# Kernel tuning notes

Measured on AMD Instinct MI355X. Metric: run time of the kernel, lower is better.

The kernel has to match this reference:

```python
import jax, jax.numpy as jnp
import numpy as np

B, S, N, D = 4, 12, 716, 64
H = 4            # num_heads
ALPHA = 0.2      # LeakyReLU negative slope
NEG = -9e15      # mask fill value from the torch code (-9000000000000000.0)


def setup_inputs() -> dict:
    key = jax.random.key(0)
    ks = jax.random.split(key, 20)
    sc = 1.0 / np.sqrt(D)
    inputs = jax.random.normal(ks[0], (B, S, N, D), dtype=jnp.float32)
    adj = jax.random.randint(ks[1], (N, N), 0, 2).astype(jnp.int32)
    in_degree = jax.random.randint(ks[2], (N,), 0, N)
    out_degree = jax.random.randint(ks[3], (N,), 0, N)
    # embeddings with padding_idx=0 -> row 0 zeroed
    in_emb = (jax.random.normal(ks[4], (N, D)) * sc).at[0].set(0.0)
    out_emb = (jax.random.normal(ks[5], (N, D)) * sc).at[0].set(0.0)
    # GAT params
    W = jax.random.normal(ks[6], (D, D)) * sc
    a1 = jax.random.normal(ks[7], (D, 1)) * sc
    a2 = jax.random.normal(ks[8], (D, 1)) * sc
    # spatial multi-head attention params
    Wq = jax.random.normal(ks[9], (D, D)) * sc
    bq = jnp.zeros((D,))
    Wk = jax.random.normal(ks[10], (D, D)) * sc
    bk = jnp.zeros((D,))
    Wv = jax.random.normal(ks[11], (D, D)) * sc
    bv = jnp.zeros((D,))
    Wo = jax.random.normal(ks[12], (D, D)) * sc
    bo = jnp.zeros((D,))
    # pred_linear: 2D -> D
    Wp = jax.random.normal(ks[13], (2 * D, D)) * (1.0 / np.sqrt(2 * D))
    bp = jnp.zeros((D,))
    return dict(inputs=inputs, adj=adj, in_degree=in_degree, out_degree=out_degree,
                in_emb=in_emb, out_emb=out_emb, W=W, a1=a1, a2=a2,
                Wq=Wq, bq=bq, Wk=Wk, bk=bk, Wv=Wv, bv=bv, Wo=Wo, bo=bo,
                Wp=Wp, bp=bp)


def reference(inputs, adj, in_degree, out_degree, in_emb, out_emb,
              W, a1, a2, Wq, bq, Wk, bk, Wv, bv, Wo, bo, Wp, bp):
    b, s, n, d = inputs.shape
    dh = d // H
    # degree embeddings, broadcast over batch & time: [N, D]
    spatial_emb = in_emb[in_degree] + out_emb[out_degree]

    # ---- GAT, vectorized over all batch*seq samples (orig loops per sample) ----
    x = inputs.reshape(b * s, n, d)
    Wh = jnp.einsum('bnd,de->bne', x, W)                 # [BS, N, D]
    Wh1 = Wh @ a1                                        # [BS, N, 1]
    Wh2 = Wh @ a2                                        # [BS, N, 1]
    e = Wh1 + jnp.swapaxes(Wh2, 1, 2)                    # [BS, N, N]
    e = jnp.where(e > 0, e, ALPHA * e)                   # LeakyReLU
    e = jnp.where(adj[None] > 0, e, NEG)                 # adjacency mask
    attn = jax.nn.softmax(e, axis=-1)                    # softmax(dim=1) on 2D == last axis
    out1 = jax.nn.elu(attn @ Wh).reshape(b, s, n, d)     # dropout is identity in eval

    # ---- Spatial multi-head attention over nodes ----
    y = inputs + spatial_emb                             # [B, S, N, D]
    q = (y @ Wq + bq).reshape(b, s, n, H, dh)
    k = (y @ Wk + bk).reshape(b, s, n, H, dh)
    v = (y @ Wv + bv).reshape(b, s, n, H, dh)
    scores = jnp.einsum('bsnhk,bsmhk->bshnm', q, k) / jnp.sqrt(jnp.float32(dh))
    p = jax.nn.softmax(scores, axis=-1)                  # [B, S, H, N, N]
    o = jnp.einsum('bshnm,bsmhk->bsnhk', p, v).reshape(b, s, n, d)
    out2 = o @ Wo + bo

    # ---- fuse and project ----
    return jnp.concatenate([out1, out2], axis=-1) @ Wp + bp
```

## Files before the change

kernel.cpp:

```cpp
#include <hip/hip_runtime.h>
#include <hip/hip_bf16.h>

#define BN   716
#define BD   64
#define BH   4
#define BDH  16
#define BBS  48
#define NCH  23
#define NJT  45

typedef __hip_bfloat16 bf16;
typedef __attribute__((ext_vector_type(8))) short short8;
typedef __attribute__((ext_vector_type(4))) short s16x4;
typedef __attribute__((ext_vector_type(4))) float f32x4;

__device__ __forceinline__ float b2f(bf16 x){ return __bfloat162float(x); }
__device__ __forceinline__ bf16 f2b(float x){ return __float2bfloat16(x); }
__device__ __forceinline__ short bfbits(float x){
  union { bf16 h; short s; } c; c.h = __float2bfloat16(x); return c.s;
}
__device__ __forceinline__ unsigned packbf(float a, float b){
  unsigned ua = __float_as_uint(a) + 0x8000u;
  unsigned ub = __float_as_uint(b) + 0x8000u;
  return __builtin_amdgcn_perm(ub, ua, 0x07060302u);
}
__device__ __forceinline__ short8 pack8(float a,float b,float c,float d,
                                        float e,float f,float g,float h){
  short8 r; r[0]=bfbits(a); r[1]=bfbits(b); r[2]=bfbits(c); r[3]=bfbits(d);
  r[4]=bfbits(e); r[5]=bfbits(f); r[6]=bfbits(g); r[7]=bfbits(h); return r;
}

#define MFMA16(a,b,c) __builtin_amdgcn_mfma_f32_16x16x32_bf16(a,b,c,0,0,0)

#if __has_builtin(__builtin_amdgcn_mfma_f32_16x16x16_bf16)
#define HAVE_MFMA16K 1
__device__ __forceinline__ f32x4 mfma16k(s16x4 a, s16x4 b, f32x4 c){
  return __builtin_amdgcn_mfma_f32_16x16x16_bf16(a, b, c, 0, 0, 0);
}
#elif __has_builtin(__builtin_amdgcn_mfma_f32_16x16x16bf16_1k)
#define HAVE_MFMA16K 1
__device__ __forceinline__ f32x4 mfma16k(s16x4 a, s16x4 b, f32x4 c){
  return __builtin_amdgcn_mfma_f32_16x16x16bf16_1k(a, b, c, 0, 0, 0);
}
#else
#define HAVE_MFMA16K 0
#endif

__global__ __launch_bounds__(256) void k_prep(
    const int* __restrict__ adj,
    const float* __restrict__ W,  const float* __restrict__ Wq,
    const float* __restrict__ Wk, const float* __restrict__ Wv,
    const float* __restrict__ Wo, const float* __restrict__ bo,
    const float* __restrict__ Wp, const float* __restrict__ bp,
    unsigned* __restrict__ mask, bf16* __restrict__ WB,
    bf16* __restrict__ WF, float* __restrict__ bfuse)
{
  int b = blockIdx.x, t = threadIdx.x;
  if (b < 65){
    int w = b * 256 + t;
    if (w < BN * NCH){
      int row = w / NCH, wc = w - row * NCH;
      unsigned m = 0;
      int jb = wc * 32;
      for (int bb = 0; bb < 32; bb++){
        int j = jb + bb;
        if (j < BN && adj[(long)row * BN + j] > 0) m |= (1u << bb);
      }
      mask[w] = m;
    }
  } else if (b < 69){
#pragma unroll
    for (int i = 0; i < 16; i++){
      int idx = (b - 65) * 4096 + i * 256 + t;
      int n = idx >> 6, kk = idx & 63;
      const float* src = (n < 64) ? W : (n < 128) ? Wq : (n < 192) ? Wk : Wv;
      WB[idx] = f2b(src[kk * BD + (n & 63)]);
    }
  } else if (b < 101){
    int idx = (b - 69) * 256 + t;
    int n = idx >> 7, kk = idx & 127;
    float v;
    if (kk < 64){
      v = Wp[kk * BD + n];
    } else {
      v = 0.f;
      int r = kk - 64;
      for (int m = 0; m < BD; m++)
        v += Wo[r * BD + m] * Wp[(BD + m) * BD + n];
    }
    WF[idx] = f2b(v);
  } else {
    if (t < BD){
      float acc = bp[t];
      for (int m = 0; m < BD; m++)
        acc += bo[m] * Wp[(BD + m) * BD + t];
      bfuse[t] = acc;
    }
  }
}

__global__ __launch_bounds__(256) void k_proj(
    const float* __restrict__ x,
    const int* __restrict__ ind, const int* __restrict__ outd,
    const float* __restrict__ in_emb, const float* __restrict__ out_emb,
    const float* __restrict__ a1p, const float* __restrict__ a2p,
    const bf16* __restrict__ WB,
    const float* __restrict__ bq, const float* __restrict__ bk, const float* __restrict__ bv,
    bf16* __restrict__ WhS, float* __restrict__ Wh1, float* __restrict__ Wh2,
    bf16* __restrict__ Qt, bf16* __restrict__ Kt, bf16* __restrict__ Vt16)
{
  __shared__ short st[64][72];
  int bs = blockIdx.x, tile = blockIdx.y;
  int n0 = tile * 64;
  int t = threadIdx.x, w = t >> 6, lane = t & 63, quad = lane >> 4, l15 = lane & 15;
  long sb = (long)bs * BN;
  int rowi = n0 + w * 16 + l15;
  int rc = rowi < BN ? rowi : BN - 1;
  const float* xr  = x + (sb + rc) * BD;
  const float* ier = in_emb  + (long)ind [rc] * BD;
  const float* oer = out_emb + (long)outd[rc] * BD;

  f32x4 aw[4], aqkv[12];
#pragma unroll
  for (int i2 = 0; i2 < 4;  i2++) aw[i2]   = (f32x4){0,0,0,0};
#pragma unroll
  for (int i2 = 0; i2 < 12; i2++) aqkv[i2] = (f32x4){0,0,0,0};

#pragma unroll
  for (int kc = 0; kc < 2; kc++){
    int k0 = kc * 32 + quad * 8;
    float4 xa = *(const float4*)(xr  + k0);
    float4 xb = *(const float4*)(xr  + k0 + 4);
    float4 ia = *(const float4*)(ier + k0);
    float4 ib = *(const float4*)(ier + k0 + 4);
    float4 oa = *(const float4*)(oer + k0);
    float4 ob = *(const float4*)(oer + k0 + 4);
    short8 ax = pack8(xa.x, xa.y, xa.z, xa.w, xb.x, xb.y, xb.z, xb.w);
    short8 ay = pack8(xa.x+ia.x+oa.x, xa.y+ia.y+oa.y, xa.z+ia.z+oa.z, xa.w+ia.w+oa.w,
                      xb.x+ib.x+ob.x, xb.y+ib.y+ob.y, xb.z+ib.z+ob.z, xb.w+ib.w+ob.w);
#pragma unroll
    for (int nt = 0; nt < 4; nt++)
      aw[nt] = MFMA16(ax, *(const short8*)(WB + (nt*16 + l15) * BD + k0), aw[nt]);
#pragma unroll
    for (int nt = 0; nt < 12; nt++)
      aqkv[nt] = MFMA16(ay, *(const short8*)(WB + (64 + nt*16 + l15) * BD + k0), aqkv[nt]);
  }

  {
    float s1v[4] = {0,0,0,0}, s2v[4] = {0,0,0,0};
#pragma unroll
    for (int nt = 0; nt < 4; nt++){
      float a1f = a1p[nt*16 + l15], a2f = a2p[nt*16 + l15];
#pragma unroll
      for (int reg = 0; reg < 4; reg++){
        s1v[reg] += aw[nt][reg] * a1f;
        s2v[reg] += aw[nt][reg] * a2f;
      }
    }
#pragma unroll
    for (int off = 1; off < 16; off <<= 1){
#pragma unroll
      for (int reg = 0; reg < 4; reg++){
        s1v[reg] += __shfl_xor(s1v[reg], off);
        s2v[reg] += __shfl_xor(s2v[reg], off);
      }
    }
    if (l15 == 0){
#pragma unroll
      for (int reg = 0; reg < 4; reg++){
        int rr = n0 + w*16 + quad*4 + reg;
        if (rr < BN){ Wh1[sb + rr] = s1v[reg]; Wh2[sb + rr] = s2v[reg]; }
      }
    }
  }

#pragma unroll
  for (int nt = 0; nt < 4; nt++)
    *(short4*)&st[nt*16 + l15][w*16 + quad*4] = make_short4(
        bfbits(aw[nt][0]), bfbits(aw[nt][1]), bfbits(aw[nt][2]), bfbits(aw[nt][3]));
  __syncthreads();
#pragma unroll
  for (int s = 0; s < 2; s++){
    int L = (t*2 + s) * 8;
    int kb = L & 31, d = (L >> 5) & 63, chl = L >> 11;
    int ch = tile * 2 + chl;
    if (ch < NCH)
      *(uint4*)(WhS + (((long)bs*NCH + ch)*64 + d)*32 + kb) = *(const uint4*)&st[d][chl*32 + kb];
  }
  __syncthreads();

#pragma unroll
  for (int nt = 0; nt < 4; nt++){
    float bb = bv[nt*16 + l15];
    *(short4*)&st[nt*16 + l15][w*16 + quad*4] = make_short4(
        bfbits(aqkv[8+nt][0]+bb), bfbits(aqkv[8+nt][1]+bb),
        bfbits(aqkv[8+nt][2]+bb), bfbits(aqkv[8+nt][3]+bb));
  }
  __syncthreads();
  {
    int jl = t >> 6;
    int c  = t & 15, qq = (t >> 4) & 3;
    int jt = tile * 4 + jl;
    if (jt < NJT){
#pragma unroll
      for (int h = 0; h < BH; h++){
        s16x4 v4 = *(const s16x4*)&st[h*16 + c][jl*16 + qq*4];
        *(s16x4*)(Vt16 + ((((long)bs*BH + h)*NJT + jt)*64 + (t & 63))*4) = v4;
      }
    }
  }
  __syncthreads();

#pragma unroll
  for (int nt = 0; nt < 4; nt++){
    float bb = bq[nt*16 + l15];
#pragma unroll
    for (int reg = 0; reg < 4; reg++)
      st[w*16 + quad*4 + reg][nt*16 + l15] = bfbits((aqkv[nt][reg] + bb) * 0.25f);
  }
  __syncthreads();
#pragma unroll
  for (int s = 0; s < 2; s++){
    int L = (t*2 + s) * 8;
    int kb = L & 15, nl = (L >> 4) & 63, h = L >> 10;
    int jt = tile * 4 + (nl >> 4);
    if (jt < NJT)
      *(uint4*)(Qt + ((((long)bs*BH + h)*NJT + jt)*16 + (nl&15))*16 + kb)
          = *(const uint4*)&st[nl][h*16 + kb];
  }
  __syncthreads();

#pragma unroll
  for (int nt = 0; nt < 4; nt++){
    float bb = bk[nt*16 + l15];
#pragma unroll
    for (int reg = 0; reg < 4; reg++)
      st[w*16 + quad*4 + reg][nt*16 + l15] = bfbits(aqkv[4+nt][reg] + bb);
  }
  __syncthreads();
#pragma unroll
  for (int s = 0; s < 2; s++){
    int L = (t*2 + s) * 8;
    int kb = L & 15, nl = (L >> 4) & 63, h = L >> 10;
    int jt = tile * 4 + (nl >> 4);
    if (jt < NJT)
      *(uint4*)(Kt + ((((long)bs*BH + h)*NJT + jt)*16 + (nl&15))*16 + kb)
          = *(const uint4*)&st[nl][h*16 + kb];
  }
}

__global__ __launch_bounds__(256) void k_attn(
    const float* __restrict__ Wh1, const float* __restrict__ Wh2,
    const unsigned* __restrict__ mask, const bf16* __restrict__ WhS,
    const bf16* __restrict__ Qt, const bf16* __restrict__ Kt,
    const bf16* __restrict__ Vt16,
    bf16* __restrict__ out1, bf16* __restrict__ o)
{
#if !HAVE_MFMA16K
  __shared__ short pw[4][16][48];
#endif
  int bs = blockIdx.x, yb = blockIdx.y;
  int t = threadIdx.x, w = t >> 6, lane = t & 63, quad = lane >> 4, l15 = lane & 15;
  long sb = (long)bs * BN;

  if (yb < 12){
    int rt = yb * 4 + w;
    if (rt >= NJT) return;
    int i = rt * 16 + l15;
    int ic = i < BN ? i : BN - 1;
    float e1 = Wh1[sb + ic];
    const unsigned* mrow = mask + (long)ic * NCH;
    const float* w2 = Wh2 + sb;

    float sl = 0.f;
    f32x4 acc0 = {0,0,0,0}, acc1 = {0,0,0,0}, acc2 = {0,0,0,0}, acc3 = {0,0,0,0};
    for (int ch = 0; ch < NCH; ch++){
      int j0 = ch * 32 + quad * 8;
      unsigned m8 = (mrow[ch] >> (quad * 8)) & 0xFFu;
      float4 wa  = *(const float4*)(w2 + j0);
      float4 wb4 = *(const float4*)(w2 + j0 + 4);
      float sv[8] = {wa.x, wa.y, wa.z, wa.w, wb4.x, wb4.y, wb4.z, wb4.w};
      float p[8];
#pragma unroll
      for (int jj = 0; jj < 8; jj++){
        float e = e1 + sv[jj];
        e = (e > 0.f) ? e : 0.2f * e;
        float pp = ((m8 >> jj) & 1u) ? __expf(e) : 0.f;
        sl += pp;
        p[jj] = pp;
      }
      union { unsigned u[4]; short8 v; } A;
      A.u[0] = packbf(p[0], p[1]); A.u[1] = packbf(p[2], p[3]);
      A.u[2] = packbf(p[4], p[5]); A.u[3] = packbf(p[6], p[7]);
      const bf16* wbp = WhS + ((long)bs*NCH + ch)*2048 + quad * 8;
      acc0 = MFMA16(A.v, *(const short8*)(wbp + ( 0 + l15) * 32), acc0);
      acc1 = MFMA16(A.v, *(const short8*)(wbp + (16 + l15) * 32), acc1);
      acc2 = MFMA16(A.v, *(const short8*)(wbp + (32 + l15) * 32), acc2);
      acc3 = MFMA16(A.v, *(const short8*)(wbp + (48 + l15) * 32), acc3);
    }
    sl += __shfl_xor(sl, 16);
    sl += __shfl_xor(sl, 32);
    float inv[4];
#pragma unroll
    for (int reg = 0; reg < 4; reg++){
      int srcl = quad * 4 + reg;
      float s = __int_as_float(__builtin_amdgcn_ds_bpermute(srcl << 2, __float_as_int(sl)));
      inv[reg] = 1.0f / s;
    }
    const f32x4* accs[4] = {&acc0, &acc1, &acc2, &acc3};
#pragma unroll
    for (int nt = 0; nt < 4; nt++){
#pragma unroll
      for (int reg = 0; reg < 4; reg++){
        int gi = rt * 16 + quad * 4 + reg;
        if (gi < BN){
          float val = (*accs[nt])[reg] * inv[reg];
          val = (val > 0.f) ? val : (__expf(val) - 1.f);
          out1[(sb + gi) * BD + nt*16 + l15] = f2b(val);
        }
      }
    }
    return;
  }

  int rt = yb - 12, h = w;
  const bf16* Qh = Qt   + ((long)bs*BH + h) * NJT * 256;
  const bf16* Kh = Kt   + ((long)bs*BH + h) * NJT * 256;
  const bf16* Vh = Vt16 + ((long)bs*BH + h) * NJT * 256;

  short8 bq = {0,0,0,0,0,0,0,0};
  if (quad < 2) bq = *(const short8*)(Qh + rt*256 + l15*16 + quad*8);

  f32x4 oacc = {0,0,0,0};
  float psum = 0.f;

#if HAVE_MFMA16K
#pragma unroll 3
  for (int jt = 0; jt < NJT; jt++){
    short8 ak = {0,0,0,0,0,0,0,0};
    if (quad < 2) ak = *(const short8*)(Kh + jt*256 + l15*16 + quad*8);
    f32x4 c = MFMA16(ak, bq, ((f32x4){0,0,0,0}));
    bool inval = (jt == NJT-1) && (quad == 3);
    float p[4];
#pragma unroll
    for (int reg = 0; reg < 4; reg++){
      float pp = __expf(c[reg]);
      pp = inval ? 0.f : pp;
      psum += pp;
      p[reg] = pp;
    }
    union { unsigned u[2]; s16x4 v; } A;
    A.u[0] = packbf(p[0], p[1]); A.u[1] = packbf(p[2], p[3]);
    s16x4 bv = *(const s16x4*)(Vh + jt*256 + lane*4);
    oacc = mfma16k(A.v, bv, oacc);
  }
#else
  for (int ch = 0; ch < NCH; ch++){
#pragma unroll
    for (int tt = 0; tt < 2; tt++){
      int jt = 2*ch + tt;
      if (jt < NJT){
        short8 ak = {0,0,0,0,0,0,0,0};
        if (quad < 2) ak = *(const short8*)(Kh + jt*256 + l15*16 + quad*8);
        f32x4 c = MFMA16(ak, bq, ((f32x4){0,0,0,0}));
        bool inval = (jt == NJT-1) && (quad == 3);
#pragma unroll
        for (int reg = 0; reg < 4; reg++){
          float pp = __expf(c[reg]);
          pp = inval ? 0.f : pp;
          psum += pp;
          pw[h][l15][tt*16 + quad*4 + reg] = (short)((__float_as_uint(pp) + 0x8000u) >> 16);
        }
      } else {
#pragma unroll
        for (int reg = 0; reg < 4; reg++) pw[h][l15][tt*16 + quad*4 + reg] = 0;
      }
    }
    short8 ap = *(const short8*)&pw[h][l15][quad*8];
    int jB = 2*ch + (quad >> 1);
    s16x4 v0 = {0,0,0,0}, v1 = {0,0,0,0};
    if (jB < NJT){
      v0 = *(const s16x4*)(Vh + jB*256 + (((quad&1)*2  )*16 + l15)*4);
      v1 = *(const s16x4*)(Vh + jB*256 + (((quad&1)*2+1)*16 + l15)*4);
    }
    short8 bv8; bv8[0]=v0[0]; bv8[1]=v0[1]; bv8[2]=v0[2]; bv8[3]=v0[3];
    bv8[4]=v1[0]; bv8[5]=v1[1]; bv8[6]=v1[2]; bv8[7]=v1[3];
    oacc = MFMA16(ap, bv8, oacc);
  }
#endif

  psum += __shfl_xor(psum, 16);
  psum += __shfl_xor(psum, 32);
#pragma unroll
  for (int reg = 0; reg < 4; reg++){
    int srcl = quad * 4 + reg;
    float s = __int_as_float(__builtin_amdgcn_ds_bpermute(srcl << 2, __float_as_int(psum)));
    int grow = rt * 16 + srcl;
    if (grow < BN)
      o[(sb + grow) * BD + h * BDH + l15] = f2b(oacc[reg] / s);
  }
}

__global__ __launch_bounds__(256) void k_final(
    const bf16* __restrict__ out1, const bf16* __restrict__ o,
    const bf16* __restrict__ WF, const float* __restrict__ bfuse,
    float* __restrict__ out)
{
  int t = threadIdx.x, w = t >> 6, lane = t & 63, quad = lane >> 4, l15 = lane & 15;
  long r0 = (long)blockIdx.x * 64;
  long row = r0 + w * 16 + l15;
  const bf16* o1r = out1 + row * BD;
  const bf16* oor = o    + row * BD;
  f32x4 acc[4];
#pragma unroll
  for (int i2 = 0; i2 < 4; i2++) acc[i2] = (f32x4){0,0,0,0};
#pragma unroll
  for (int kc = 0; kc < 2; kc++){
    int k0 = kc * 32 + quad * 8;
    short8 a1 = *(const short8*)(o1r + k0);
    short8 a2 = *(const short8*)(oor + k0);
#pragma unroll
    for (int nt = 0; nt < 4; nt++){
      acc[nt] = MFMA16(a1, *(const short8*)(WF + (nt*16 + l15) * 128 + k0), acc[nt]);
      acc[nt] = MFMA16(a2, *(const short8*)(WF + (nt*16 + l15) * 128 + 64 + k0), acc[nt]);
    }
  }
#pragma unroll
  for (int nt = 0; nt < 4; nt++){
    float bf = bfuse[nt*16 + l15];
#pragma unroll
    for (int reg = 0; reg < 4; reg++)
      out[(r0 + w*16 + quad*4 + reg) * BD + nt*16 + l15] = acc[nt][reg] + bf;
  }
}

extern "C" void kernel_launch(void* const* d_in, const int* in_sizes, int n_in,
                              void* d_out, int out_size, void* d_ws, size_t ws_size,
                              hipStream_t stream){
  const float* inp    = (const float*)d_in[0];
  const int*   adj    = (const int*)  d_in[1];
  const int*   ind    = (const int*)  d_in[2];
  const int*   outd   = (const int*)  d_in[3];
  const float* in_emb = (const float*)d_in[4];
  const float* out_emb= (const float*)d_in[5];
  const float* W      = (const float*)d_in[6];
  const float* a1     = (const float*)d_in[7];
  const float* a2     = (const float*)d_in[8];
  const float* Wq     = (const float*)d_in[9];
  const float* bq     = (const float*)d_in[10];
  const float* Wk     = (const float*)d_in[11];
  const float* bk     = (const float*)d_in[12];
  const float* Wv     = (const float*)d_in[13];
  const float* bv     = (const float*)d_in[14];
  const float* Wo     = (const float*)d_in[15];
  const float* bo     = (const float*)d_in[16];
  const float* Wp     = (const float*)d_in[17];
  const float* bp     = (const float*)d_in[18];

  const long PER  = (long)BBS * BN * BD;
  const long WHS  = (long)BBS * NCH * 64 * 32;
  const long QTS  = (long)BBS * BH * NJT * 16 * 16;
  bf16* WhSb  = (bf16*)d_ws;
  bf16* Vt16b = WhSb  + WHS;
  bf16* Qtb   = Vt16b + QTS;
  bf16* Ktb   = Qtb   + QTS;
  bf16* o1B   = Ktb   + QTS;
  bf16* oB    = o1B + PER;
  bf16* WBb   = oB  + PER;
  bf16* WFb   = WBb + 256 * BD;
  unsigned* maskb = (unsigned*)(WFb + BD * 128);
  float* fws  = (float*)(maskb + BN * NCH);
  float* Wh1  = fws;
  float* Wh2  = Wh1 + (long)BBS * BN + 64;
  float* bfuse= Wh2 + (long)BBS * BN + 64;

  hipLaunchKernelGGL(k_prep, dim3(102), dim3(256), 0, stream,
                     adj, W, Wq, Wk, Wv, Wo, bo, Wp, bp,
                     maskb, WBb, WFb, bfuse);
  hipLaunchKernelGGL(k_proj, dim3(BBS, 12), dim3(256), 0, stream,
                     inp, ind, outd, in_emb, out_emb, a1, a2, WBb, bq, bk, bv,
                     WhSb, Wh1, Wh2, Qtb, Ktb, Vt16b);
  hipLaunchKernelGGL(k_attn, dim3(BBS, 57), dim3(256), 0, stream,
                     Wh1, Wh2, maskb, WhSb, Qtb, Ktb, Vt16b, o1B, oB);
  hipLaunchKernelGGL(k_final, dim3(537), dim3(256), 0, stream,
                     o1B, oB, WFb, bfuse, (float*)d_out);
}
```

Measured before the change: 177.4 us.

## Factor GAT exponentials, fold log2e into Q scale, process two query tiles per wave

```diff
diff --git a/kernel.cpp b/kernel.cpp
--- a/kernel.cpp
+++ b/kernel.cpp
@@ -8,6 +8,7 @@
 #define BBS  48
 #define NCH  23
 #define NJT  45
+#define QSCALE 0.3606737602f
 
 typedef __hip_bfloat16 bf16;
 typedef __attribute__((ext_vector_type(8))) short short8;
@@ -28,6 +29,20 @@
                                         float e,float f,float g,float h){
   short8 r; r[0]=bfbits(a); r[1]=bfbits(b); r[2]=bfbits(c); r[3]=bfbits(d);
   r[4]=bfbits(e); r[5]=bfbits(f); r[6]=bfbits(g); r[7]=bfbits(h); return r;
+}
+__device__ __forceinline__ float fexp2(float x){
+#if __has_builtin(__builtin_amdgcn_exp2f)
+  return __builtin_amdgcn_exp2f(x);
+#else
+  return __expf(x * 0.6931471805599453f);
+#endif
+}
+__device__ __forceinline__ float frcp(float x){
+#if __has_builtin(__builtin_amdgcn_rcpf)
+  return __builtin_amdgcn_rcpf(x);
+#else
+  return 1.0f / x;
+#endif
 }
 
 #define MFMA16(a,b,c) __builtin_amdgcn_mfma_f32_16x16x32_bf16(a,b,c,0,0,0)
@@ -106,7 +121,7 @@
     const float* __restrict__ a1p, const float* __restrict__ a2p,
     const bf16* __restrict__ WB,
     const float* __restrict__ bq, const float* __restrict__ bk, const float* __restrict__ bv,
-    bf16* __restrict__ WhS, float* __restrict__ Wh1, float* __restrict__ Wh2,
+    bf16* __restrict__ WhS, float* __restrict__ Wh1, float2* __restrict__ EwP,
     bf16* __restrict__ Qt, bf16* __restrict__ Kt, bf16* __restrict__ Vt16)
 {
   __shared__ short st[64][72];
@@ -169,7 +184,11 @@
 #pragma unroll
       for (int reg = 0; reg < 4; reg++){
         int rr = n0 + w*16 + quad*4 + reg;
-        if (rr < BN){ Wh1[sb + rr] = s1v[reg]; Wh2[sb + rr] = s2v[reg]; }
+        if (rr < BN){
+          Wh1[sb + rr] = s1v[reg];
+          float s2 = s2v[reg];
+          EwP[sb + rr] = make_float2(__expf(s2), __expf(0.2f * s2));
+        }
       }
     }
   }
@@ -216,7 +235,7 @@
     float bb = bq[nt*16 + l15];
 #pragma unroll
     for (int reg = 0; reg < 4; reg++)
-      st[w*16 + quad*4 + reg][nt*16 + l15] = bfbits((aqkv[nt][reg] + bb) * 0.25f);
+      st[w*16 + quad*4 + reg][nt*16 + l15] = bfbits((aqkv[nt][reg] + bb) * QSCALE);
   }
   __syncthreads();
 #pragma unroll
@@ -250,7 +269,7 @@
 }
 
 __global__ __launch_bounds__(256) void k_attn(
-    const float* __restrict__ Wh1, const float* __restrict__ Wh2,
+    const float* __restrict__ Wh1, const float2* __restrict__ EwP,
     const unsigned* __restrict__ mask, const bf16* __restrict__ WhS,
     const bf16* __restrict__ Qt, const bf16* __restrict__ Kt,
     const bf16* __restrict__ Vt16,
@@ -269,23 +288,27 @@
     int i = rt * 16 + l15;
     int ic = i < BN ? i : BN - 1;
     float e1 = Wh1[sb + ic];
+    float Aa = __expf(e1), Cc = __expf(0.2f * e1);
+    float invA = frcp(Aa);
     const unsigned* mrow = mask + (long)ic * NCH;
-    const float* w2 = Wh2 + sb;
+    const float2* ew = EwP + sb;
 
     float sl = 0.f;
     f32x4 acc0 = {0,0,0,0}, acc1 = {0,0,0,0}, acc2 = {0,0,0,0}, acc3 = {0,0,0,0};
     for (int ch = 0; ch < NCH; ch++){
       int j0 = ch * 32 + quad * 8;
       unsigned m8 = (mrow[ch] >> (quad * 8)) & 0xFFu;
-      float4 wa  = *(const float4*)(w2 + j0);
-      float4 wb4 = *(const float4*)(w2 + j0 + 4);
-      float sv[8] = {wa.x, wa.y, wa.z, wa.w, wb4.x, wb4.y, wb4.z, wb4.w};
+      const float4* ef = (const float4*)(ew + j0);
+      float4 q0 = ef[0], q1 = ef[1], q2 = ef[2], q3 = ef[3];
+      float Bv[8] = {q0.x, q0.z, q1.x, q1.z, q2.x, q2.z, q3.x, q3.z};
+      float Dv[8] = {q0.y, q0.w, q1.y, q1.w, q2.y, q2.w, q3.y, q3.w};
       float p[8];
 #pragma unroll
       for (int jj = 0; jj < 8; jj++){
-        float e = e1 + sv[jj];
-        e = (e > 0.f) ? e : 0.2f * e;
-        float pp = ((m8 >> jj) & 1u) ? __expf(e) : 0.f;
+        bool cond = Bv[jj] > invA;
+        float f = cond ? Bv[jj] : Dv[jj];
+        float g = cond ? Aa : Cc;
+        float pp = ((m8 >> jj) & 1u) ? f * g : 0.f;
         sl += pp;
         p[jj] = pp;
       }
@@ -323,81 +346,99 @@
     return;
   }
 
-  int rt = yb - 12, h = w;
+  int h = w;
+  int rt0 = (yb - 12) * 2, rt1 = rt0 + 1;
   const bf16* Qh = Qt   + ((long)bs*BH + h) * NJT * 256;
   const bf16* Kh = Kt   + ((long)bs*BH + h) * NJT * 256;
   const bf16* Vh = Vt16 + ((long)bs*BH + h) * NJT * 256;
 
-  short8 bq = {0,0,0,0,0,0,0,0};
-  if (quad < 2) bq = *(const short8*)(Qh + rt*256 + l15*16 + quad*8);
-
-  f32x4 oacc = {0,0,0,0};
-  float psum = 0.f;
+  short8 aq0 = {0,0,0,0,0,0,0,0}, aq1 = {0,0,0,0,0,0,0,0};
+  if (quad < 2){
+    aq0 = *(const short8*)(Qh + rt0*256 + l15*16 + quad*8);
+    aq1 = *(const short8*)(Qh + rt1*256 + l15*16 + quad*8);
+  }
+  f32x4 o0 = {0,0,0,0}, o1 = {0,0,0,0};
+  float ps0 = 0.f, ps1 = 0.f;
 
 #if HAVE_MFMA16K
-#pragma unroll 3
-  for (int jt = 0; jt < NJT; jt++){
+  auto step = [&](int jt, bool tail){
     short8 ak = {0,0,0,0,0,0,0,0};
     if (quad < 2) ak = *(const short8*)(Kh + jt*256 + l15*16 + quad*8);
-    f32x4 c = MFMA16(ak, bq, ((f32x4){0,0,0,0}));
-    bool inval = (jt == NJT-1) && (quad == 3);
-    float p[4];
+    f32x4 c0 = MFMA16(ak, aq0, ((f32x4){0,0,0,0}));
+    f32x4 c1 = MFMA16(ak, aq1, ((f32x4){0,0,0,0}));
+    float p0[4], p1[4];
 #pragma unroll
     for (int reg = 0; reg < 4; reg++){
-      float pp = __expf(c[reg]);
-      pp = inval ? 0.f : pp;
-      psum += pp;
-      p[reg] = pp;
-    }
-    union { unsigned u[2]; s16x4 v; } A;
-    A.u[0] = packbf(p[0], p[1]); A.u[1] = packbf(p[2], p[3]);
+      float a = fexp2(c0[reg]);
+      float b = fexp2(c1[reg]);
+      if (tail && quad == 3){ a = 0.f; b = 0.f; }
+      ps0 += a; ps1 += b;
+      p0[reg] = a; p1[reg] = b;
+    }
+    union { unsigned u[2]; s16x4 v; } A0, A1;
+    A0.u[0] = packbf(p0[0], p0[1]); A0.u[1] = packbf(p0[2], p0[3]);
+    A1.u[0] = packbf(p1[0], p1[1]); A1.u[1] = packbf(p1[2], p1[3]);
     s16x4 bv = *(const s16x4*)(Vh + jt*256 + lane*4);
-    oacc = mfma16k(A.v, bv, oacc);
-  }
+    o0 = mfma16k(A0.v, bv, o0);
+    o1 = mfma16k(A1.v, bv, o1);
+  };
+  for (int jt = 0; jt < NJT - 1; jt++) step(jt, false);
+  step(NJT - 1, true);
 #else
-  for (int ch = 0; ch < NCH; ch++){
-#pragma unroll
-    for (int tt = 0; tt < 2; tt++){
-      int jt = 2*ch + tt;
-      if (jt < NJT){
-        short8 ak = {0,0,0,0,0,0,0,0};
-        if (quad < 2) ak = *(const short8*)(Kh + jt*256 + l15*16 + quad*8);
-        f32x4 c = MFMA16(ak, bq, ((f32x4){0,0,0,0}));
-        bool inval = (jt == NJT-1) && (quad == 3);
-#pragma unroll
-        for (int reg = 0; reg < 4; reg++){
-          float pp = __expf(c[reg]);
-          pp = inval ? 0.f : pp;
-          psum += pp;
-          pw[h][l15][tt*16 + quad*4 + reg] = (short)((__float_as_uint(pp) + 0x8000u) >> 16);
+  for (int pass = 0; pass < 2; pass++){
+    int rt = pass ? rt1 : rt0;
+    short8 aq = pass ? aq1 : aq0;
+    f32x4 oacc = {0,0,0,0};
+    float psum = 0.f;
+    if (rt < NJT){
+      for (int ch = 0; ch < NCH; ch++){
+#pragma unroll
+        for (int tt = 0; tt < 2; tt++){
+          int jt = 2*ch + tt;
+          if (jt < NJT){
+            short8 ak = {0,0,0,0,0,0,0,0};
+            if (quad < 2) ak = *(const short8*)(Kh + jt*256 + l15*16 + quad*8);
+            f32x4 c = MFMA16(ak, aq, ((f32x4){0,0,0,0}));
+            bool inval = (jt == NJT-1) && (quad == 3);
+#pragma unroll
+            for (int reg = 0; reg < 4; reg++){
+              float pp = fexp2(c[reg]);
+              pp = inval ? 0.f : pp;
+              psum += pp;
+              pw[h][l15][tt*16 + quad*4 + reg] = (short)((__float_as_uint(pp) + 0x8000u) >> 16);
+            }
+          } else {
+#pragma unroll
+            for (int reg = 0; reg < 4; reg++) pw[h][l15][tt*16 + quad*4 + reg] = 0;
+          }
         }
-      } else {
-#pragma unroll
-        for (int reg = 0; reg < 4; reg++) pw[h][l15][tt*16 + quad*4 + reg] = 0;
-      }
-    }
-    short8 ap = *(const short8*)&pw[h][l15][quad*8];
-    int jB = 2*ch + (quad >> 1);
-    s16x4 v0 = {0,0,0,0}, v1 = {0,0,0,0};
-    if (jB < NJT){
-      v0 = *(const s16x4*)(Vh + jB*256 + (((quad&1)*2  )*16 + l15)*4);
-      v1 = *(const s16x4*)(Vh + jB*256 + (((quad&1)*2+1)*16 + l15)*4);
-    }
-    short8 bv8; bv8[0]=v0[0]; bv8[1]=v0[1]; bv8[2]=v0[2]; bv8[3]=v0[3];
-    bv8[4]=v1[0]; bv8[5]=v1[1]; bv8[6]=v1[2]; bv8[7]=v1[3];
-    oacc = MFMA16(ap, bv8, oacc);
+        short8 ap = *(const short8*)&pw[h][l15][quad*8];
+        int jB = 2*ch + (quad >> 1);
+        s16x4 v0 = {0,0,0,0}, v1 = {0,0,0,0};
+        if (jB < NJT){
+          v0 = *(const s16x4*)(Vh + jB*256 + (((quad&1)*2  )*16 + l15)*4);
+          v1 = *(const s16x4*)(Vh + jB*256 + (((quad&1)*2+1)*16 + l15)*4);
+        }
+        short8 bv8; bv8[0]=v0[0]; bv8[1]=v0[1]; bv8[2]=v0[2]; bv8[3]=v0[3];
+        bv8[4]=v1[0]; bv8[5]=v1[1]; bv8[6]=v1[2]; bv8[7]=v1[3];
+        oacc = MFMA16(ap, bv8, oacc);
+      }
+    }
+    if (pass){ o1 = oacc; ps1 = psum; } else { o0 = oacc; ps0 = psum; }
   }
 #endif
 
-  psum += __shfl_xor(psum, 16);
-  psum += __shfl_xor(psum, 32);
+  ps0 += __shfl_xor(ps0, 16); ps0 += __shfl_xor(ps0, 32);
+  ps1 += __shfl_xor(ps1, 16); ps1 += __shfl_xor(ps1, 32);
 #pragma unroll
   for (int reg = 0; reg < 4; reg++){
     int srcl = quad * 4 + reg;
-    float s = __int_as_float(__builtin_amdgcn_ds_bpermute(srcl << 2, __float_as_int(psum)));
-    int grow = rt * 16 + srcl;
-    if (grow < BN)
-      o[(sb + grow) * BD + h * BDH + l15] = f2b(oacc[reg] / s);
+    float s0 = __int_as_float(__builtin_amdgcn_ds_bpermute(srcl << 2, __float_as_int(ps0)));
+    float s1 = __int_as_float(__builtin_amdgcn_ds_bpermute(srcl << 2, __float_as_int(ps1)));
+    int g0 = rt0 * 16 + srcl;
+    int g1 = rt1 * 16 + srcl;
+    if (g0 < BN) o[(sb + g0) * BD + h * BDH + l15] = f2b(o0[reg] / s0);
+    if (g1 < BN) o[(sb + g1) * BD + h * BDH + l15] = f2b(o1[reg] / s1);
   }
 }
 
@@ -469,19 +510,19 @@
   bf16* WBb   = oB  + PER;
   bf16* WFb   = WBb + 256 * BD;
   unsigned* maskb = (unsigned*)(WFb + BD * 128);
-  float* fws  = (float*)(maskb + BN * NCH);
+  float2* EwPb = (float2*)(maskb + BN * NCH);
+  float* fws  = (float*)(EwPb + (long)BBS * BN + 32);
   float* Wh1  = fws;
-  float* Wh2  = Wh1 + (long)BBS * BN + 64;
-  float* bfuse= Wh2 + (long)BBS * BN + 64;
+  float* bfuse= Wh1 + (long)BBS * BN + 64;
 
   hipLaunchKernelGGL(k_prep, dim3(102), dim3(256), 0, stream,
                      adj, W, Wq, Wk, Wv, Wo, bo, Wp, bp,
                      maskb, WBb, WFb, bfuse);
   hipLaunchKernelGGL(k_proj, dim3(BBS, 12), dim3(256), 0, stream,
                      inp, ind, outd, in_emb, out_emb, a1, a2, WBb, bq, bk, bv,
-                     WhSb, Wh1, Wh2, Qtb, Ktb, Vt16b);
-  hipLaunchKernelGGL(k_attn, dim3(BBS, 57), dim3(256), 0, stream,
-                     Wh1, Wh2, maskb, WhSb, Qtb, Ktb, Vt16b, o1B, oB);
+                     WhSb, Wh1, EwPb, Qtb, Ktb, Vt16b);
+  hipLaunchKernelGGL(k_attn, dim3(BBS, 35), dim3(256), 0, stream,
+                     Wh1, EwPb, maskb, WhSb, Qtb, Ktb, Vt16b, o1B, oB);
   hipLaunchKernelGGL(k_final, dim3(537), dim3(256), 0, stream,
                      o1B, oB, WFb, bfuse, (float*)d_out);
 }
```

After: 178.6 us. No clear change (+0.7%).
